# Kernel tuning notes

Hardware: AMD Instinct MI355X
Metric: run time of the kernel (lower is better)

The kernel has to match this reference:

```python
import jax, jax.numpy as jnp
import numpy as np

N = 100000      # num nodes
C = 48          # feature / label dim
E = 1600000     # num edges (avg in-degree 16)
M = 20000       # num labeled nodes
L = 10          # diffusion_layer
LAM = 0.9       # lambda_


def setup_inputs() -> dict:
    key = jax.random.key(0)
    k1, k2, k3, k4, k5 = jax.random.split(key, 5)
    Z = jax.random.normal(k1, (N, C), dtype=jnp.float32)
    Y = jax.random.uniform(k2, (M, C), dtype=jnp.float32)
    mask = jax.random.randint(k3, (M,), 0, N, dtype=jnp.int32)
    # ensure every node has in-degree >= 1 so deg**-0.5 stays finite
    row = jax.random.randint(k4, (E,), 0, N, dtype=jnp.int32)
    col = jnp.concatenate([jnp.arange(N, dtype=jnp.int32),
                           jax.random.randint(k5, (E - N,), 0, N, dtype=jnp.int32)])
    edge_index = jnp.stack([row, col])  # [2, E]
    return {"Z": Z, "Y": Y, "mask": mask, "edge_index": edge_index, "beta": 0}


def reference(Z, Y, mask, edge_index, beta):
    num_nodes = Z.shape[0]
    # G = Z.clone(); G[mask] = Y   (noise=False branch is identity)
    G = Z.at[mask].set(Y)
    row, col = edge_index[0], edge_index[1]
    # degree_vector = sparse.sum(adj, 0)  -> column sums (in-degree), duplicates accumulate
    deg = jax.ops.segment_sum(jnp.ones(col.shape, Z.dtype), col, num_segments=num_nodes)
    dinv = deg ** -0.5
    # normalized edge weights of D^{-1/2} A D^{-1/2}
    w = dinv[row] * dinv[col]  # [E]

    def step(x, _):
        # x <- lambda * (adj @ x) + (1 - lambda) * G
        agg = jax.ops.segment_sum(w[:, None] * x[col], row, num_segments=num_nodes)
        return agg * LAM + (1.0 - LAM) * G, None

    x, _ = jax.lax.scan(step, G, None, length=L)
    return x
```

## Files before the change

### kernel.cpp

```cpp
#include <hip/hip_runtime.h>
#include <hip/hip_fp16.h>

#define FEAT 48
#define CH 12
#define STEPS 10
#define BK 256
#define NBMAX 512
#define CAP 5120
constexpr float LAM   = 0.9f;
constexpr float OMLAM = 0.1f;


__global__ void init_kernel(int* __restrict__ bcur, int* __restrict__ ccur, int nb) {
    int b = blockIdx.x * blockDim.x + threadIdx.x;
    if (b < nb) { bcur[b] = b * CAP; ccur[b] = b * CAP; }
}

__global__ void winner_kernel(const int* __restrict__ mask, int* __restrict__ winner, int M) {
    int i = blockIdx.x * blockDim.x + threadIdx.x;
    if (i < M) atomicMax(&winner[mask[i]], i);
}

__global__ void bucket_scatter(const int* __restrict__ row, const int* __restrict__ col,
                               int* __restrict__ bcur, int* __restrict__ ccur,
                               int2* __restrict__ bstore, int* __restrict__ cstore,
                               int E, int nb, int nblk) {
    __shared__ int hr[NBMAX], cr[NBMAX], hc[NBMAX], cc[NBMAX];
    int tid = threadIdx.x;
    int ce = (E + nblk - 1) / nblk;
    int s = blockIdx.x * ce;
    int e_end = min(E, s + ce);
    for (int i = tid; i < nb; i += blockDim.x) { hr[i] = 0; hc[i] = 0; }
    __syncthreads();
    for (int i = s + tid; i < e_end; i += blockDim.x) {
        atomicAdd(&hr[row[i] >> 8], 1);
        atomicAdd(&hc[col[i] >> 8], 1);
    }
    __syncthreads();
    for (int i = tid; i < nb; i += blockDim.x) {
        cr[i] = hr[i] ? atomicAdd(&bcur[i], hr[i]) : 0;
        cc[i] = hc[i] ? atomicAdd(&ccur[i], hc[i]) : 0;
    }
    __syncthreads();
    for (int i = s + tid; i < e_end; i += blockDim.x) {
        int r = row[i], c = col[i];
        int pr = atomicAdd(&cr[r >> 8], 1);
        bstore[pr] = make_int2(r, c);
        int pc = atomicAdd(&cc[c >> 8], 1);
        cstore[pc] = c;
    }
}

__global__ void bucket_prefix(const int* __restrict__ bcur, int* __restrict__ bpre,
                              int* __restrict__ off, int nb, int E, int N) {
    __shared__ int sh[NBMAX];
    int tid = threadIdx.x;
    int tot = (tid < nb) ? (bcur[tid] - tid * CAP) : 0;
    sh[tid] = tot;
    __syncthreads();
    for (int d = 1; d < NBMAX; d <<= 1) {
        int v = (tid >= d) ? sh[tid - d] : 0;
        __syncthreads();
        sh[tid] += v;
        __syncthreads();
    }
    if (tid < nb) bpre[tid] = sh[tid] - tot;
    if (tid == 0) off[N] = E;
}

__global__ void csr_finish(const int2* __restrict__ bstore, const int* __restrict__ bcur,
                           const int* __restrict__ bpre, int* __restrict__ off,
                           int* __restrict__ csr_col, int N) {
    __shared__ int h[BK], loc[BK], cur[BK];
    int b = blockIdx.x, tid = threadIdx.x;
    int cnt  = bcur[b] - b * CAP;
    int base = bpre[b];
    const int2* src = bstore + (size_t)b * CAP;
    h[tid] = 0;
    __syncthreads();
    for (int i = tid; i < cnt; i += BK) atomicAdd(&h[src[i].x & (BK - 1)], 1);
    __syncthreads();
    int v = h[tid];
    loc[tid] = v;
    __syncthreads();
    for (int d = 1; d < BK; d <<= 1) {
        int t = (tid >= d) ? loc[tid - d] : 0;
        __syncthreads();
        loc[tid] += t;
        __syncthreads();
    }
    int excl = loc[tid] - v;
    int r = b * BK + tid;
    if (r < N) off[r] = base + excl;
    cur[tid] = excl;
    __syncthreads();
    for (int i = tid; i < cnt; i += BK) {
        int2 e = src[i];
        int p = atomicAdd(&cur[e.x & (BK - 1)], 1);
        csr_col[base + p] = e.y;
    }
}

__global__ void deg_finish(const int* __restrict__ cstore, const int* __restrict__ ccur,
                           float* __restrict__ dinv, int N) {
    __shared__ int h[BK];
    int b = blockIdx.x, tid = threadIdx.x;
    int cnt = ccur[b] - b * CAP;
    const int* src = cstore + (size_t)b * CAP;
    h[tid] = 0;
    __syncthreads();
    for (int i = tid; i < cnt; i += BK) atomicAdd(&h[src[i] & (BK - 1)], 1);
    __syncthreads();
    int c = b * BK + tid;
    if (c < N) dinv[c] = (float)(1.0 / sqrt((double)h[tid]));
}

__global__ void prep_kernel(const float4* __restrict__ Z4, const float4* __restrict__ Y4,
                            const int* __restrict__ winner, const float* __restrict__ dinv,
                            float4* __restrict__ G4, uint2* __restrict__ u0, int N) {
    int t = blockIdx.x * blockDim.x + threadIdx.x;
    if (t >= N * CH) return;
    int r = t / CH, q = t - r * CH;
    int w = winner[r];
    float4 g = (w >= 0) ? Y4[(size_t)w * CH + q] : Z4[t];
    G4[t] = g;
    float d = dinv[r];
    __half2 h0 = __floats2half2_rn(d * g.x, d * g.y);
    __half2 h1 = __floats2half2_rn(d * g.z, d * g.w);
    u0[t] = make_uint2(__builtin_bit_cast(unsigned int, h0),
                       __builtin_bit_cast(unsigned int, h1));
}

template<bool LAST>
__global__ void diffuse_kernel(const uint2* __restrict__ up, const uint2* __restrict__ u0,
                               const float* __restrict__ dinv, const float4* __restrict__ G4,
                               const int* __restrict__ off, const int* __restrict__ cols,
                               uint2* __restrict__ uout, float4* __restrict__ xout, int N) {
    int t = blockIdx.x * blockDim.x + threadIdx.x;
    if (t >= N * CH) return;
    int r = t / CH, q = t - r * CH;
    int j0 = off[r], j1 = off[r + 1];
    float ax = 0.f, ay = 0.f, az = 0.f, aw = 0.f;

    int j = j0;
    for (; j + 4 <= j1; j += 4) {
        int c0 = cols[j], c1 = cols[j + 1], c2 = cols[j + 2], c3 = cols[j + 3];
        uint2 v0 = up[(size_t)c0 * CH + q];
        uint2 v1 = up[(size_t)c1 * CH + q];
        uint2 v2 = up[(size_t)c2 * CH + q];
        uint2 v3 = up[(size_t)c3 * CH + q];
        float2 f;
        f = __half22float2(__builtin_bit_cast(__half2, v0.x)); ax += f.x; ay += f.y;
        f = __half22float2(__builtin_bit_cast(__half2, v0.y)); az += f.x; aw += f.y;
        f = __half22float2(__builtin_bit_cast(__half2, v1.x)); ax += f.x; ay += f.y;
        f = __half22float2(__builtin_bit_cast(__half2, v1.y)); az += f.x; aw += f.y;
        f = __half22float2(__builtin_bit_cast(__half2, v2.x)); ax += f.x; ay += f.y;
        f = __half22float2(__builtin_bit_cast(__half2, v2.y)); az += f.x; aw += f.y;
        f = __half22float2(__builtin_bit_cast(__half2, v3.x)); ax += f.x; ay += f.y;
        f = __half22float2(__builtin_bit_cast(__half2, v3.y)); az += f.x; aw += f.y;
    }
    if (j < j1) {
        int c0 = cols[j];
        int c1 = (j + 1 < j1) ? cols[j + 1] : c0;
        int c2 = (j + 2 < j1) ? cols[j + 2] : c0;
        uint2 v0 = up[(size_t)c0 * CH + q];
        uint2 v1 = up[(size_t)c1 * CH + q];
        uint2 v2 = up[(size_t)c2 * CH + q];
        float2 f;
        f = __half22float2(__builtin_bit_cast(__half2, v0.x)); ax += f.x; ay += f.y;
        f = __half22float2(__builtin_bit_cast(__half2, v0.y)); az += f.x; aw += f.y;
        if (j + 1 < j1) {
            f = __half22float2(__builtin_bit_cast(__half2, v1.x)); ax += f.x; ay += f.y;
            f = __half22float2(__builtin_bit_cast(__half2, v1.y)); az += f.x; aw += f.y;
        }
        if (j + 2 < j1) {
            f = __half22float2(__builtin_bit_cast(__half2, v2.x)); ax += f.x; ay += f.y;
            f = __half22float2(__builtin_bit_cast(__half2, v2.y)); az += f.x; aw += f.y;
        }
    }

    float d = dinv[r];
    if (LAST) {
        float4 g = G4[t];
        float4 o;
        float s = LAM * d;
        o.x = fmaf(s, ax, OMLAM * g.x);
        o.y = fmaf(s, ay, OMLAM * g.y);
        o.z = fmaf(s, az, OMLAM * g.z);
        o.w = fmaf(s, aw, OMLAM * g.w);
        xout[t] = o;
    } else {
        float a = LAM * d * d;
        uint2 z = u0[t];
        float2 b0 = __half22float2(__builtin_bit_cast(__half2, z.x));
        float2 b1 = __half22float2(__builtin_bit_cast(__half2, z.y));
        __half2 h0 = __floats2half2_rn(fmaf(a, ax, OMLAM * b0.x),
                                       fmaf(a, ay, OMLAM * b0.y));
        __half2 h1 = __floats2half2_rn(fmaf(a, az, OMLAM * b1.x),
                                       fmaf(a, aw, OMLAM * b1.y));
        uout[t] = make_uint2(__builtin_bit_cast(unsigned int, h0),
                             __builtin_bit_cast(unsigned int, h1));
    }
}


extern "C" void kernel_launch(void* const* d_in, const int* in_sizes, int n_in,
                              void* d_out, int out_size, void* d_ws, size_t ws_size,
                              hipStream_t stream) {
    const float* Z    = (const float*)d_in[0];
    const float* Y    = (const float*)d_in[1];
    const int*   mask = (const int*)d_in[2];
    const int*   ei   = (const int*)d_in[3];

    const int N = in_sizes[0] / FEAT;
    const int M = in_sizes[2];
    const int E = in_sizes[3] / 2;
    const int* row = ei;
    const int* col = ei + E;
    const int NB = (N + BK - 1) / BK;

    char* ws = (char*)d_ws;
    size_t pos = 0;
    auto alloc = [&](size_t bytes) -> void* {
        void* p = ws + pos;
        pos = (pos + bytes + 255) & ~(size_t)255;
        return p;
    };
    float* G      = (float*)alloc((size_t)N * FEAT * 4);
    uint2* u0     = (uint2*)alloc((size_t)N * CH * 8);
    uint2* ua     = (uint2*)alloc((size_t)N * CH * 8);
    uint2* ub     = (uint2*)alloc((size_t)N * CH * 8);
    float* dinv   = (float*)alloc((size_t)N * 4);
    int*   off    = (int*)  alloc((size_t)(N + 1) * 4);
    int*   winner = (int*)  alloc((size_t)N * 4);
    int*   csr    = (int*)  alloc((size_t)E * 4);
    int2*  bstore = (int2*) alloc((size_t)NB * CAP * 8);
    int*   cstore = (int*)  alloc((size_t)NB * CAP * 4);
    int*   bcur   = (int*)  alloc((size_t)NBMAX * 4);
    int*   ccur   = (int*)  alloc((size_t)NBMAX * 4);
    int*   bpre   = (int*)  alloc((size_t)NBMAX * 4);

    hipMemsetAsync(winner, 0xFF, (size_t)N * 4, stream);

    const int B = 256;
    init_kernel  <<<(NB + B - 1) / B, B, 0, stream>>>(bcur, ccur, NB);
    winner_kernel<<<(M + B - 1) / B, B, 0, stream>>>(mask, winner, M);

    const int SBLK = 256;
    bucket_scatter<<<SBLK, B, 0, stream>>>(row, col, bcur, ccur, bstore, cstore, E, NB, SBLK);
    bucket_prefix <<<1, NBMAX, 0, stream>>>(bcur, bpre, off, NB, E, N);
    csr_finish    <<<NB, BK, 0, stream>>>(bstore, bcur, bpre, off, csr, N);
    deg_finish    <<<NB, BK, 0, stream>>>(cstore, ccur, dinv, N);

    prep_kernel<<<(N * CH + B - 1) / B, B, 0, stream>>>((const float4*)Z, (const float4*)Y,
                                                        winner, dinv, (float4*)G, u0, N);

    const int nt = N * CH;
    const uint2* src = u0;
    uint2* bufs[2] = { ua, ub };
    for (int it = 0; it < STEPS - 1; ++it) {
        uint2* dst = bufs[it & 1];
        diffuse_kernel<false><<<(nt + B - 1) / B, B, 0, stream>>>(
            src, u0, dinv, (const float4*)G, off, csr, dst, nullptr, N);
        src = dst;
    }
    diffuse_kernel<true><<<(nt + B - 1) / B, B, 0, stream>>>(
        src, u0, dinv, (const float4*)G, off, csr, nullptr, (float4*)d_out, N);
}
```

Baseline: 444.4 us.

## Pack bucket staging entries, merge setup and finish kernels, widen scatter blocks

The staged bucket entries are packed so each CSR entry is a 32-bit word (column shifted left plus the low row bits) and each degree entry is a single byte, instead of int2 and int. This cuts staging write and read traffic. The init and winner kernels are merged into one launch, csr_finish and deg_finish become one kernel, and the bucket scatter now runs 1024 threads per block. The packing assumes column indices fit in 24 bits. Larger scatter blocks raise contention on the shared-memory atomics.

```diff
diff --git a/kernel.cpp b/kernel.cpp
--- a/kernel.cpp
+++ b/kernel.cpp
@@ -11,20 +11,18 @@
 constexpr float OMLAM = 0.1f;
 
 
-__global__ void init_kernel(int* __restrict__ bcur, int* __restrict__ ccur, int nb) {
-    int b = blockIdx.x * blockDim.x + threadIdx.x;
-    if (b < nb) { bcur[b] = b * CAP; ccur[b] = b * CAP; }
-}
-
-__global__ void winner_kernel(const int* __restrict__ mask, int* __restrict__ winner, int M) {
+__global__ void setup_kernel(int* __restrict__ bcur, int* __restrict__ ccur, int nb,
+                             const int* __restrict__ mask, int* __restrict__ winner, int M) {
     int i = blockIdx.x * blockDim.x + threadIdx.x;
+    if (i < nb) { bcur[i] = i * CAP; ccur[i] = i * CAP; }
     if (i < M) atomicMax(&winner[mask[i]], i);
 }
 
-__global__ void bucket_scatter(const int* __restrict__ row, const int* __restrict__ col,
-                               int* __restrict__ bcur, int* __restrict__ ccur,
-                               int2* __restrict__ bstore, int* __restrict__ cstore,
-                               int E, int nb, int nblk) {
+__global__ __launch_bounds__(1024)
+void bucket_scatter(const int* __restrict__ row, const int* __restrict__ col,
+                    int* __restrict__ bcur, int* __restrict__ ccur,
+                    unsigned int* __restrict__ bstore, unsigned char* __restrict__ cstore,
+                    int E, int nb, int nblk) {
     __shared__ int hr[NBMAX], cr[NBMAX], hc[NBMAX], cc[NBMAX];
     int tid = threadIdx.x;
     int ce = (E + nblk - 1) / nblk;
@@ -45,9 +43,9 @@
     for (int i = s + tid; i < e_end; i += blockDim.x) {
         int r = row[i], c = col[i];
         int pr = atomicAdd(&cr[r >> 8], 1);
-        bstore[pr] = make_int2(r, c);
+        bstore[pr] = ((unsigned int)c << 8) | (unsigned int)(r & (BK - 1));
         int pc = atomicAdd(&cc[c >> 8], 1);
-        cstore[pc] = c;
+        cstore[pc] = (unsigned char)(c & (BK - 1));
     }
 }
 
@@ -68,17 +66,20 @@
     if (tid == 0) off[N] = E;
 }
 
-__global__ void csr_finish(const int2* __restrict__ bstore, const int* __restrict__ bcur,
-                           const int* __restrict__ bpre, int* __restrict__ off,
-                           int* __restrict__ csr_col, int N) {
+__global__ void finish_kernel(const unsigned int* __restrict__ bstore,
+                              const int* __restrict__ bcur, const int* __restrict__ bpre,
+                              const unsigned char* __restrict__ cstore,
+                              const int* __restrict__ ccur,
+                              int* __restrict__ off, int* __restrict__ csr_col,
+                              float* __restrict__ dinv, int N) {
     __shared__ int h[BK], loc[BK], cur[BK];
     int b = blockIdx.x, tid = threadIdx.x;
     int cnt  = bcur[b] - b * CAP;
     int base = bpre[b];
-    const int2* src = bstore + (size_t)b * CAP;
+    const unsigned int* src = bstore + (size_t)b * CAP;
     h[tid] = 0;
     __syncthreads();
-    for (int i = tid; i < cnt; i += BK) atomicAdd(&h[src[i].x & (BK - 1)], 1);
+    for (int i = tid; i < cnt; i += BK) atomicAdd(&h[src[i] & (BK - 1)], 1);
     __syncthreads();
     int v = h[tid];
     loc[tid] = v;
@@ -95,21 +96,16 @@
     cur[tid] = excl;
     __syncthreads();
     for (int i = tid; i < cnt; i += BK) {
-        int2 e = src[i];
-        int p = atomicAdd(&cur[e.x & (BK - 1)], 1);
-        csr_col[base + p] = e.y;
-    }
-}
-
-__global__ void deg_finish(const int* __restrict__ cstore, const int* __restrict__ ccur,
-                           float* __restrict__ dinv, int N) {
-    __shared__ int h[BK];
-    int b = blockIdx.x, tid = threadIdx.x;
-    int cnt = ccur[b] - b * CAP;
-    const int* src = cstore + (size_t)b * CAP;
+        unsigned int e = src[i];
+        int p = atomicAdd(&cur[e & (BK - 1)], 1);
+        csr_col[base + p] = (int)(e >> 8);
+    }
+    __syncthreads();
     h[tid] = 0;
     __syncthreads();
-    for (int i = tid; i < cnt; i += BK) atomicAdd(&h[src[i] & (BK - 1)], 1);
+    int ccnt = ccur[b] - b * CAP;
+    const unsigned char* csrc = cstore + (size_t)b * CAP;
+    for (int i = tid; i < ccnt; i += BK) atomicAdd(&h[csrc[i]], 1);
     __syncthreads();
     int c = b * BK + tid;
     if (c < N) dinv[c] = (float)(1.0 / sqrt((double)h[tid]));
@@ -234,8 +230,8 @@
     int*   off    = (int*)  alloc((size_t)(N + 1) * 4);
     int*   winner = (int*)  alloc((size_t)N * 4);
     int*   csr    = (int*)  alloc((size_t)E * 4);
-    int2*  bstore = (int2*) alloc((size_t)NB * CAP * 8);
-    int*   cstore = (int*)  alloc((size_t)NB * CAP * 4);
+    unsigned int*  bstore = (unsigned int*) alloc((size_t)NB * CAP * 4);
+    unsigned char* cstore = (unsigned char*)alloc((size_t)NB * CAP);
     int*   bcur   = (int*)  alloc((size_t)NBMAX * 4);
     int*   ccur   = (int*)  alloc((size_t)NBMAX * 4);
     int*   bpre   = (int*)  alloc((size_t)NBMAX * 4);
@@ -243,14 +239,14 @@
     hipMemsetAsync(winner, 0xFF, (size_t)N * 4, stream);
 
     const int B = 256;
-    init_kernel  <<<(NB + B - 1) / B, B, 0, stream>>>(bcur, ccur, NB);
-    winner_kernel<<<(M + B - 1) / B, B, 0, stream>>>(mask, winner, M);
+    const int setup_n = max(NB, M);
+    setup_kernel<<<(setup_n + B - 1) / B, B, 0, stream>>>(bcur, ccur, NB, mask, winner, M);
 
     const int SBLK = 256;
-    bucket_scatter<<<SBLK, B, 0, stream>>>(row, col, bcur, ccur, bstore, cstore, E, NB, SBLK);
+    bucket_scatter<<<SBLK, 1024, 0, stream>>>(row, col, bcur, ccur, bstore, cstore, E, NB, SBLK);
     bucket_prefix <<<1, NBMAX, 0, stream>>>(bcur, bpre, off, NB, E, N);
-    csr_finish    <<<NB, BK, 0, stream>>>(bstore, bcur, bpre, off, csr, N);
-    deg_finish    <<<NB, BK, 0, stream>>>(cstore, ccur, dinv, N);
+    finish_kernel <<<NB, BK, 0, stream>>>(bstore, bcur, bpre, cstore, ccur,
+                                          off, csr, dinv, N);
 
     prep_kernel<<<(N * CH + B - 1) / B, B, 0, stream>>>((const float4*)Z, (const float4*)Y,
                                                         winner, dinv, (float4*)G, u0, N);
```

After: 427.4 us. 1.04x faster.
